# Kernel optimization log

Measured on AMD Instinct MI355X. Metric: run time of the kernel, lower is better.

The kernel has to match this reference:

```python
import jax, jax.numpy as jnp
import numpy as np

DIM = 768
HID = 1536
EPS = 1e-12
SCALE = float(np.sqrt(DIM))


def _layernorm(x, gamma, beta):
    mu = jnp.mean(x, axis=-1, keepdims=True)
    var = jnp.mean(jnp.square(x - mu), axis=-1, keepdims=True)
    return (x - mu) * jax.lax.rsqrt(var + EPS) * gamma + beta


def setup_inputs() -> dict:
    key = jax.random.key(0)
    ks = jax.random.split(key, 16)
    s = 1.0 / np.sqrt(DIM)
    sh = 1.0 / np.sqrt(HID)
    x = jax.random.normal(ks[0], (8, 2048, DIM), dtype=jnp.float32)
    return {
        "x": x,
        "Wq": jax.random.uniform(ks[1], (DIM, DIM), jnp.float32, -s, s),
        "bq": jax.random.uniform(ks[2], (DIM,), jnp.float32, -s, s),
        "Wk": jax.random.uniform(ks[3], (DIM, DIM), jnp.float32, -s, s),
        "bk": jax.random.uniform(ks[4], (DIM,), jnp.float32, -s, s),
        "Wv": jax.random.uniform(ks[5], (DIM, DIM), jnp.float32, -s, s),
        "bv": jax.random.uniform(ks[6], (DIM,), jnp.float32, -s, s),
        "Wp": jax.random.uniform(ks[7], (DIM, DIM), jnp.float32, -s, s),
        "bp": jax.random.uniform(ks[8], (DIM,), jnp.float32, -s, s),
        "g1": jnp.ones((DIM,), jnp.float32),
        "be1": jnp.zeros((DIM,), jnp.float32),
        "W1": jax.random.uniform(ks[9], (HID, DIM), jnp.float32, -s, s),
        "b1": jax.random.uniform(ks[10], (HID,), jnp.float32, -s, s),
        "W2": jax.random.uniform(ks[11], (DIM, HID), jnp.float32, -sh, sh),
        "b2": jax.random.uniform(ks[12], (DIM,), jnp.float32, -sh, sh),
        "g2": jnp.ones((DIM,), jnp.float32),
        "be2": jnp.zeros((DIM,), jnp.float32),
    }


def reference(x, Wq, bq, Wk, bk, Wv, bv, Wp, bp, g1, be1, W1, b1, W2, b2, g2, be2):
    # NOTE: original code does NOT split into heads; single full-dim bmm attention.
    Q = jnp.einsum("bsd,ed->bse", x, Wq) + bq  # [B,S,D]
    K = jnp.einsum("bsd,ed->bse", x, Wk) + bk
    V = jnp.einsum("bsd,ed->bse", x, Wv) + bv
    alpha = jnp.einsum("bqd,bkd->bqk", Q, K) / SCALE  # [B,S,S]
    alpha = jax.nn.softmax(alpha, axis=-1)
    attn = jnp.einsum("bqk,bkd->bqd", alpha, V)
    attn = jnp.einsum("bsd,ed->bse", attn, Wp) + bp  # linear_proj
    h = _layernorm(x + attn, g1, be1)
    mlp = jax.nn.gelu(jnp.einsum("bsd,hd->bsh", h, W1) + b1, approximate=False)
    mlp = jnp.einsum("bsh,dh->bsd", mlp, W2) + b2
    return _layernorm(h + mlp, g2, be2)
```

## Files before the change

### kernel.cpp

```cpp
#include <hip/hip_runtime.h>
#include <math.h>

#define D_MODEL 768
#define D_HID   1536
#define N_BATCH 8
#define SEQLEN  2048
#define NROWS   (N_BATCH*SEQLEN)

typedef unsigned short u16;
typedef __attribute__((ext_vector_type(8))) short bfrag;
typedef __attribute__((ext_vector_type(4))) float facc;

__device__ __forceinline__ u16 f2bf(float f) {
  unsigned u = __float_as_uint(f);
  u += 0x7fffu + ((u >> 16) & 1u);
  return (u16)(u >> 16);
}
__device__ __forceinline__ float bf2f(u16 u) {
  return __uint_as_float((unsigned)u << 16);
}

__device__ __forceinline__ void async16(const void* g, void* l) {
  __builtin_amdgcn_global_load_lds((const __attribute__((address_space(1))) void*)g,
                                   (__attribute__((address_space(3))) void*)l,
                                   16, 0, 0);
}

__global__ __launch_bounds__(256) void cvt_all(
    const float* __restrict__ x,  const float* __restrict__ Wq,
    const float* __restrict__ Wk, const float* __restrict__ Wv,
    const float* __restrict__ Wp, const float* __restrict__ W1,
    const float* __restrict__ W2, const float* __restrict__ bq,
    const float* __restrict__ bk, const float* __restrict__ bv,
    u16* __restrict__ XB, u16* __restrict__ WQKV, u16* __restrict__ WPB,
    u16* __restrict__ W1B, u16* __restrict__ W2B, float* __restrict__ BQKV) {
  long i = (long)blockIdx.x * 256 + threadIdx.x;
  const float* src; u16* dst; long off;
  if      (i < 3145728) { src = x;  dst = XB;             off = i; }
  else if (i < 3293184) { src = Wq; dst = WQKV;           off = i - 3145728; }
  else if (i < 3440640) { src = Wk; dst = WQKV + 589824;  off = i - 3293184; }
  else if (i < 3588096) { src = Wv; dst = WQKV + 1179648; off = i - 3440640; }
  else if (i < 3735552) { src = Wp; dst = WPB;            off = i - 3588096; }
  else if (i < 4030464) { src = W1; dst = W1B;            off = i - 3735552; }
  else if (i < 4325376) { src = W2; dst = W2B;            off = i - 4030464; }
  else if (i < 4325952) {
    long j = i - 4325376;
    const float* s = (j < 192) ? bq : (j < 384) ? bk : bv;
    long o = (j < 192) ? j : (j < 384) ? j - 192 : j - 384;
    ((float4*)BQKV)[j] = ((const float4*)s)[o];
    return;
  } else return;
  float4 v = ((const float4*)src)[off];
  ushort4 o4;
  o4.x = f2bf(v.x); o4.y = f2bf(v.y); o4.z = f2bf(v.z); o4.w = f2bf(v.w);
  *reinterpret_cast<ushort4*>(dst + off * 4) = o4;
}

enum { EPI_EXP = 1, EPI_DIV = 2, EPI_GELU = 4, EPI_QKV = 5, EPI_RES = 6 };

template<int EPI>
__global__ __launch_bounds__(512, 4)
void gemm_bt(const u16* __restrict__ Aall, const u16* __restrict__ Ball,
             void* __restrict__ Cout,
             int M, int N, int K,
             long sA, long sB, long sC,
             const float* __restrict__ bias,
             const u16* __restrict__ resid,
             float* __restrict__ lsum,
             float scale)
{
  __shared__ __align__(16) char smem[65536];
  u16* As = (u16*)smem;
  u16* Bs = (u16*)(smem + 16384);

  const int z = blockIdx.z;
  const u16* A = Aall + (long)z * sA;
  const u16* B = Ball + (long)z * sB;
  const int bm = blockIdx.x, bn = blockIdx.y;
  const int tid = (int)threadIdx.x;
  const int lane = tid & 63, wv = tid >> 6;
  const int wr = wv >> 2, wc = wv & 3;

  facc acc[4][4] = {};

  const int srow = tid >> 3;
  const int scol = (((tid & 7) ^ (srow & 7)) << 3);
  const u16* Abase = A + (long)(bm * 128) * K;
  const u16* Bbase = B + (long)(bn * 256) * K;

  const int fr = lane & 15;
  const int g0 = lane >> 4;

  for (int k0 = 0; k0 < K; k0 += 64) {
    __syncthreads();
#pragma unroll
    for (int p = 0; p < 2; ++p)
      async16(Abase + (long)(p * 64 + srow) * K + k0 + scol, As + (p * 512 + wv * 64) * 8);
#pragma unroll
    for (int p = 0; p < 4; ++p)
      async16(Bbase + (long)(p * 64 + srow) * K + k0 + scol, Bs + (p * 512 + wv * 64) * 8);
    __syncthreads();
#pragma unroll
    for (int h = 0; h < 2; ++h) {
      bfrag af[4], bfv[4];
      const int gh = g0 + h * 4;
#pragma unroll
      for (int i = 0; i < 4; ++i) {
        const int r = wr * 64 + i * 16 + fr;
        af[i] = *(const bfrag*)(As + r * 64 + ((gh ^ (r & 7)) << 3));
      }
#pragma unroll
      for (int j = 0; j < 4; ++j) {
        const int r = wc * 64 + j * 16 + fr;
        bfv[j] = *(const bfrag*)(Bs + r * 64 + ((gh ^ (r & 7)) << 3));
      }
#pragma unroll
      for (int i = 0; i < 4; ++i)
#pragma unroll
        for (int j = 0; j < 4; ++j)
          acc[i][j] = __builtin_amdgcn_mfma_f32_16x16x32_bf16(af[i], bfv[j], acc[i][j], 0, 0, 0);
    }
  }

  __syncthreads();
  const int rb = bm * 128 + wr * 64;
  const int cb = bn * 256 + wc * 64;
  const int quad = lane >> 4;

  if constexpr (EPI == EPI_QKV) {
    const int c64 = bn * 4 + wc;
    const int which = c64 / 12;
    float bj[4];
#pragma unroll
    for (int j = 0; j < 4; ++j) bj[j] = bias[cb + j * 16 + fr];
    if (which == 2) {
      u16* VT_ = (u16*)resid;
      const int zb = rb >> 11;
      const int seqb = (rb & 2047) + quad * 4;
      const int dimb = (c64 - 24) * 64;
#pragma unroll
      for (int i = 0; i < 4; ++i) {
#pragma unroll
        for (int j = 0; j < 4; ++j) {
          const int dim = dimb + j * 16 + fr;
          ushort4 o;
          o.x = f2bf(acc[i][j][0] + bj[j]);
          o.y = f2bf(acc[i][j][1] + bj[j]);
          o.z = f2bf(acc[i][j][2] + bj[j]);
          o.w = f2bf(acc[i][j][3] + bj[j]);
          *reinterpret_cast<ushort4*>(VT_ + (long)zb * D_MODEL * SEQLEN +
                                      (long)dim * SEQLEN + seqb + i * 16) = o;
        }
      }
      return;
    }
    u16* ep16 = (u16*)(smem + wv * 8192);
    u16* Cg = (u16*)Cout + (long)which * NROWS * D_MODEL;
    const int cbo = (c64 - which * 12) * 64;
#pragma unroll
    for (int i = 0; i < 4; ++i)
#pragma unroll
      for (int r = 0; r < 4; ++r) {
        const int lrow = i * 16 + quad * 4 + r;
#pragma unroll
        for (int j = 0; j < 4; ++j)
          ep16[lrow * 64 + j * 16 + fr] = f2bf(acc[i][j][r] + bj[j]);
      }
#pragma unroll
    for (int it = 0; it < 8; ++it) {
      const int lr = it * 8 + (lane >> 3);
      const int ch = (lane & 7) << 3;
      int4 d = *(const int4*)(ep16 + lr * 64 + ch);
      *reinterpret_cast<int4*>(Cg + (long)(rb + lr) * D_MODEL + cbo + ch) = d;
    }
  } else {
    u16* ep16 = (u16*)(smem + wv * 8192);
    u16* Cg = (u16*)Cout + (long)z * sC;
    float bj[4];
    if constexpr (EPI == EPI_GELU) {
#pragma unroll
      for (int j = 0; j < 4; ++j) bj[j] = bias[cb + j * 16 + fr];
    }
#pragma unroll
    for (int i = 0; i < 4; ++i) {
#pragma unroll
      for (int r = 0; r < 4; ++r) {
        const int lrow = i * 16 + quad * 4 + r;
        const int row = rb + lrow;
        float rs = 0.f;
#pragma unroll
        for (int j = 0; j < 4; ++j) {
          float v = acc[i][j][r];
          float outv;
          if constexpr (EPI == EPI_EXP) {
            outv = __expf(v * scale);
            rs += outv;
          } else {
            float t = v + bj[j];
            outv = 0.5f * t * (1.f + erff(t * 0.70710678f));
          }
          ep16[lrow * 64 + j * 16 + fr] = f2bf(outv);
        }
        if constexpr (EPI == EPI_EXP) {
          rs += __shfl_xor(rs, 1);
          rs += __shfl_xor(rs, 2);
          rs += __shfl_xor(rs, 4);
          rs += __shfl_xor(rs, 8);
          if (fr == 0) atomicAdd(&lsum[(long)z * M + row], rs);
        }
      }
    }
#pragma unroll
    for (int it = 0; it < 8; ++it) {
      const int lr = it * 8 + (lane >> 3);
      const int ch = (lane & 7) << 3;
      int4 d = *(const int4*)(ep16 + lr * 64 + ch);
      *reinterpret_cast<int4*>(Cg + (long)(rb + lr) * N + cb + ch) = d;
    }
  }
}

template<int EPI>
__global__ __launch_bounds__(256, 4)
void gemm_bt128(const u16* __restrict__ Aall, const u16* __restrict__ Ball,
                void* __restrict__ Cout,
                int M, int N, int K,
                long sA, long sB, long sC,
                const float* __restrict__ bias,
                const u16* __restrict__ resid,
                float* __restrict__ lsum,
                float scale)
{
  __shared__ __align__(16) char smem[32768];
  u16* As = (u16*)smem;
  u16* Bs = (u16*)(smem + 16384);

  const int z = blockIdx.z;
  const u16* A = Aall + (long)z * sA;
  const u16* B = Ball + (long)z * sB;
  const int bm = blockIdx.x, bn = blockIdx.y;
  const int tid = (int)threadIdx.x;
  const int lane = tid & 63, wv = tid >> 6;
  const int wr = wv >> 1, wc = wv & 1;

  facc acc[4][4] = {};

  const int srow = tid >> 3;
  const int scol = (((tid & 7) ^ (srow & 7)) << 3);
  const u16* Abase = A + (long)(bm * 128) * K;
  const u16* Bbase = B + (long)(bn * 128) * K;
  const int fr = lane & 15, g0 = lane >> 4;

  for (int k0 = 0; k0 < K; k0 += 64) {
    __syncthreads();
#pragma unroll
    for (int p = 0; p < 4; ++p) {
      async16(Abase + (long)(p * 32 + srow) * K + k0 + scol, As + (p * 256 + wv * 64) * 8);
      async16(Bbase + (long)(p * 32 + srow) * K + k0 + scol, Bs + (p * 256 + wv * 64) * 8);
    }
    __syncthreads();
#pragma unroll
    for (int h = 0; h < 2; ++h) {
      bfrag af[4], bfv[4];
      const int gh = g0 + h * 4;
#pragma unroll
      for (int i = 0; i < 4; ++i) {
        const int r = wr * 64 + i * 16 + fr;
        af[i] = *(const bfrag*)(As + r * 64 + ((gh ^ (r & 7)) << 3));
      }
#pragma unroll
      for (int j = 0; j < 4; ++j) {
        const int r = wc * 64 + j * 16 + fr;
        bfv[j] = *(const bfrag*)(Bs + r * 64 + ((gh ^ (r & 7)) << 3));
      }
#pragma unroll
      for (int i = 0; i < 4; ++i)
#pragma unroll
        for (int j = 0; j < 4; ++j)
          acc[i][j] = __builtin_amdgcn_mfma_f32_16x16x32_bf16(af[i], bfv[j], acc[i][j], 0, 0, 0);
    }
  }

  __syncthreads();
  const int rb = bm * 128 + wr * 64;
  const int cb = bn * 128 + wc * 64;
  const int quad = lane >> 4;

  if constexpr (EPI == EPI_RES) {
    float* ep32 = (float*)(smem + wv * 8192);
    u16* Cg = (u16*)Cout;
#pragma unroll
    for (int h = 0; h < 2; ++h) {
#pragma unroll
      for (int i2 = 0; i2 < 2; ++i2) {
        const int i = h * 2 + i2;
#pragma unroll
        for (int r = 0; r < 4; ++r) {
          const int lrow = i2 * 16 + quad * 4 + r;
#pragma unroll
          for (int j = 0; j < 4; ++j)
            ep32[lrow * 64 + j * 16 + fr] = acc[i][j][r];
        }
      }
#pragma unroll
      for (int it = 0; it < 8; ++it) {
        const int lr = it * 4 + (lane >> 4);
        const int ch = (lane & 15) << 2;
        float4 d = *(const float4*)(ep32 + lr * 64 + ch);
        const int row = rb + h * 32 + lr;
        const int gcol = cb + ch;
        const long gi = (long)row * N + gcol;
        ushort4 rv = *(const ushort4*)(resid + gi);
        float4 bb = *(const float4*)(bias + gcol);
        ushort4 o;
        o.x = f2bf(d.x + bb.x + bf2f(rv.x));
        o.y = f2bf(d.y + bb.y + bf2f(rv.y));
        o.z = f2bf(d.z + bb.z + bf2f(rv.z));
        o.w = f2bf(d.w + bb.w + bf2f(rv.w));
        *reinterpret_cast<ushort4*>(Cg + gi) = o;
      }
    }
  } else {
    u16* ep16 = (u16*)(smem + wv * 8192);
    u16* Cg = (u16*)Cout + (long)z * sC;
#pragma unroll
    for (int i = 0; i < 4; ++i) {
#pragma unroll
      for (int r = 0; r < 4; ++r) {
        const int lrow = i * 16 + quad * 4 + r;
        const int row = rb + lrow;
        const float inv = 1.f / lsum[(long)z * M + row];
#pragma unroll
        for (int j = 0; j < 4; ++j)
          ep16[lrow * 64 + j * 16 + fr] = f2bf(acc[i][j][r] * inv);
      }
    }
#pragma unroll
    for (int it = 0; it < 8; ++it) {
      const int lr = it * 8 + (lane >> 3);
      const int ch = (lane & 7) << 3;
      int4 d = *(const int4*)(ep16 + lr * 64 + ch);
      *reinterpret_cast<int4*>(Cg + (long)(rb + lr) * N + cb + ch) = d;
    }
  }
}

__global__ __launch_bounds__(192) void layernorm_rows(const u16* __restrict__ in,
                                                      const float* __restrict__ gamma,
                                                      const float* __restrict__ beta,
                                                      float* __restrict__ outf,
                                                      u16* __restrict__ outb) {
  const int row = blockIdx.x;
  const int t = threadIdx.x;
  ushort4 uv = ((const ushort4*)(in + (long)row * D_MODEL))[t];
  float v0 = bf2f(uv.x), v1 = bf2f(uv.y), v2 = bf2f(uv.z), v3 = bf2f(uv.w);
  float s1 = v0 + v1 + v2 + v3;
  float s2 = v0 * v0 + v1 * v1 + v2 * v2 + v3 * v3;
#pragma unroll
  for (int o = 32; o; o >>= 1) { s1 += __shfl_xor(s1, o); s2 += __shfl_xor(s2, o); }
  __shared__ float r1[3], r2[3];
  const int wv = t >> 6, ln = t & 63;
  if (ln == 0) { r1[wv] = s1; r2[wv] = s2; }
  __syncthreads();
  s1 = r1[0] + r1[1] + r1[2];
  s2 = r2[0] + r2[1] + r2[2];
  const float mu = s1 * (1.f / 768.f);
  const float var = s2 * (1.f / 768.f) - mu * mu;
  const float rstd = rsqrtf(var + 1e-12f);
  float4 gv = ((const float4*)gamma)[t];
  float4 bv = ((const float4*)beta)[t];
  float o0 = (v0 - mu) * rstd * gv.x + bv.x;
  float o1 = (v1 - mu) * rstd * gv.y + bv.y;
  float o2 = (v2 - mu) * rstd * gv.z + bv.z;
  float o3 = (v3 - mu) * rstd * gv.w + bv.w;
  if (outf) {
    float4 ov = {o0, o1, o2, o3};
    ((float4*)(outf + (long)row * D_MODEL))[t] = ov;
  }
  if (outb) {
    ushort4 ob;
    ob.x = f2bf(o0); ob.y = f2bf(o1); ob.z = f2bf(o2); ob.w = f2bf(o3);
    ((ushort4*)(outb + (long)row * D_MODEL))[t] = ob;
  }
}

static const size_t OFF_WP   = 0;
static const size_t OFF_W1   = 1179648;
static const size_t OFF_W2   = 3538944;
static const size_t OFF_LSUM = 5898240;
static const size_t OFF_BQKV = 5963776;
static const size_t OFF_QB   = 6291456;
static const size_t OFF_KB   = 31457280;
static const size_t OFF_VB   = 56623104;
static const size_t OFF_VT   = 81788928;
static const size_t OFF_EB   = 106954752;
static const size_t OFF_XB   = 174063616;
static const size_t OFF_WQKV = 199229440;

extern "C" void kernel_launch(void* const* d_in, const int* in_sizes, int n_in,
                              void* d_out, int out_size, void* d_ws, size_t ws_size,
                              hipStream_t stream) {
  const float* x   = (const float*)d_in[0];
  const float* Wq  = (const float*)d_in[1];
  const float* bq  = (const float*)d_in[2];
  const float* Wk  = (const float*)d_in[3];
  const float* bk  = (const float*)d_in[4];
  const float* Wv  = (const float*)d_in[5];
  const float* bv  = (const float*)d_in[6];
  const float* Wp  = (const float*)d_in[7];
  const float* bp  = (const float*)d_in[8];
  const float* g1  = (const float*)d_in[9];
  const float* be1 = (const float*)d_in[10];
  const float* W1  = (const float*)d_in[11];
  const float* b1  = (const float*)d_in[12];
  const float* W2  = (const float*)d_in[13];
  const float* b2  = (const float*)d_in[14];
  const float* g2  = (const float*)d_in[15];
  const float* be2 = (const float*)d_in[16];

  char* ws = (char*)d_ws;
  u16*   WPB  = (u16*)(ws + OFF_WP);
  u16*   W1B  = (u16*)(ws + OFF_W1);
  u16*   W2B  = (u16*)(ws + OFF_W2);
  float* LSUM = (float*)(ws + OFF_LSUM);
  float* BQKV = (float*)(ws + OFF_BQKV);
  u16*   QB   = (u16*)(ws + OFF_QB);
  u16*   KB   = (u16*)(ws + OFF_KB);
  u16*   VT   = (u16*)(ws + OFF_VT);
  u16*   EB   = (u16*)(ws + OFF_EB);
  u16*   XB   = (u16*)(ws + OFF_XB);
  u16*   WQKV = (u16*)(ws + OFF_WQKV);
  u16*   CTX  = (u16*)(ws + OFF_VB);
  u16*   PB   = (u16*)(ws + OFF_QB);
  u16*   HB   = (u16*)(ws + OFF_EB);
  u16*   M1B  = (u16*)(ws + OFF_QB);
  u16*   M2B  = (u16*)(ws + OFF_VT);

  dim3 blk(256), blkg(512), blkl(192);

  cvt_all<<<dim3(16899), blk, 0, stream>>>(x, Wq, Wk, Wv, Wp, W1, W2, bq, bk, bv,
                                           XB, WQKV, WPB, W1B, W2B, BQKV);
  hipMemsetAsync(LSUM, 0, NROWS * sizeof(float), stream);

  gemm_bt<EPI_QKV><<<dim3(128, 9, 1), blkg, 0, stream>>>(XB, WQKV, QB,
      NROWS, 3 * D_MODEL, D_MODEL, 0, 0, 0, BQKV, VT, nullptr, 0.f);

  const float sc = 1.0f / sqrtf((float)D_MODEL);
  gemm_bt<EPI_EXP><<<dim3(16, 8, 8), blkg, 0, stream>>>(QB, KB, EB,
      SEQLEN, SEQLEN, D_MODEL,
      (long)SEQLEN * D_MODEL, (long)SEQLEN * D_MODEL, (long)SEQLEN * SEQLEN,
      nullptr, nullptr, LSUM, sc);
  gemm_bt128<EPI_DIV><<<dim3(16, 6, 8), blk, 0, stream>>>(EB, VT, CTX,
      SEQLEN, D_MODEL, SEQLEN,
      (long)SEQLEN * SEQLEN, (long)D_MODEL * SEQLEN, (long)SEQLEN * D_MODEL,
      nullptr, nullptr, LSUM, 0.f);
  gemm_bt128<EPI_RES><<<dim3(128, 6, 1), blk, 0, stream>>>(CTX, WPB, PB,
      NROWS, D_MODEL, D_MODEL, 0, 0, 0, bp, XB, nullptr, 0.f);
  layernorm_rows<<<dim3(NROWS), blkl, 0, stream>>>(PB, g1, be1, nullptr, HB);
  gemm_bt<EPI_GELU><<<dim3(128, 6, 1), blkg, 0, stream>>>(HB, W1B, M1B,
      NROWS, D_HID, D_MODEL, 0, 0, 0, b1, nullptr, nullptr, 0.f);
  gemm_bt128<EPI_RES><<<dim3(128, 6, 1), blk, 0, stream>>>(M1B, W2B, M2B,
      NROWS, D_MODEL, D_HID, 0, 0, 0, b2, HB, nullptr, 0.f);
  layernorm_rows<<<dim3(NROWS), blkl, 0, stream>>>(M2B, g2, be2, (float*)d_out, nullptr);

  (void)in_sizes; (void)n_in; (void)out_size; (void)ws_size;
}
```

Baseline: 482.0 us.

## Move attention GEMMs to FP8 with new fp8 MFMA kernel and tanh GELU

Q, K, V^T and the exponentiated score matrix are stored as FP8, and a new gemm_f8 kernel runs QK^T and PV with fp8 MFMA instructions at K-step 128. This halves the bytes of the largest intermediates and should raise matrix throughput. The exact erf GELU is replaced with a tanh approximation, the LSUM memset is folded into the conversion kernel, and the exp uses a fixed offset of -3 to keep values inside FP8 range. Each of these trades accuracy for speed, and the GELU change means the code no longer computes the exact GELU the reference specifies.

```diff
diff --git a/kernel.cpp b/kernel.cpp
--- a/kernel.cpp
+++ b/kernel.cpp
@@ -8,6 +8,7 @@
 #define NROWS   (N_BATCH*SEQLEN)
 
 typedef unsigned short u16;
+typedef unsigned char  u8;
 typedef __attribute__((ext_vector_type(8))) short bfrag;
 typedef __attribute__((ext_vector_type(4))) float facc;
 
@@ -18,6 +19,9 @@
 }
 __device__ __forceinline__ float bf2f(u16 u) {
   return __uint_as_float((unsigned)u << 16);
+}
+__device__ __forceinline__ u8 f2fp8(float f) {
+  return (u8)(__builtin_amdgcn_cvt_pk_fp8_f32(f, f, 0, 0) & 0xff);
 }
 
 __device__ __forceinline__ void async16(const void* g, void* l) {
@@ -33,7 +37,8 @@
     const float* __restrict__ W2, const float* __restrict__ bq,
     const float* __restrict__ bk, const float* __restrict__ bv,
     u16* __restrict__ XB, u16* __restrict__ WQKV, u16* __restrict__ WPB,
-    u16* __restrict__ W1B, u16* __restrict__ W2B, float* __restrict__ BQKV) {
+    u16* __restrict__ W1B, u16* __restrict__ W2B, float* __restrict__ BQKV,
+    float* __restrict__ LSUM) {
   long i = (long)blockIdx.x * 256 + threadIdx.x;
   const float* src; u16* dst; long off;
   if      (i < 3145728) { src = x;  dst = XB;             off = i; }
@@ -49,6 +54,10 @@
     long o = (j < 192) ? j : (j < 384) ? j - 192 : j - 384;
     ((float4*)BQKV)[j] = ((const float4*)s)[o];
     return;
+  } else if (i < 4330048) {
+    float4 zz = {0.f, 0.f, 0.f, 0.f};
+    ((float4*)LSUM)[i - 4325952] = zz;
+    return;
   } else return;
   float4 v = ((const float4*)src)[off];
   ushort4 o4;
@@ -134,7 +143,7 @@
 #pragma unroll
     for (int j = 0; j < 4; ++j) bj[j] = bias[cb + j * 16 + fr];
     if (which == 2) {
-      u16* VT_ = (u16*)resid;
+      u8* VT_ = (u8*)resid;
       const int zb = rb >> 11;
       const int seqb = (rb & 2047) + quad * 4;
       const int dimb = (c64 - 24) * 64;
@@ -143,19 +152,19 @@
 #pragma unroll
         for (int j = 0; j < 4; ++j) {
           const int dim = dimb + j * 16 + fr;
-          ushort4 o;
-          o.x = f2bf(acc[i][j][0] + bj[j]);
-          o.y = f2bf(acc[i][j][1] + bj[j]);
-          o.z = f2bf(acc[i][j][2] + bj[j]);
-          o.w = f2bf(acc[i][j][3] + bj[j]);
-          *reinterpret_cast<ushort4*>(VT_ + (long)zb * D_MODEL * SEQLEN +
-                                      (long)dim * SEQLEN + seqb + i * 16) = o;
+          unsigned v01 = __builtin_amdgcn_cvt_pk_fp8_f32(acc[i][j][0] + bj[j],
+                                                         acc[i][j][1] + bj[j], 0, 0);
+          unsigned v23 = __builtin_amdgcn_cvt_pk_fp8_f32(acc[i][j][2] + bj[j],
+                                                         acc[i][j][3] + bj[j], 0, 0);
+          unsigned w = (v01 & 0xffffu) | (v23 << 16);
+          *reinterpret_cast<unsigned*>(VT_ + (long)zb * D_MODEL * SEQLEN +
+                                       (long)dim * SEQLEN + seqb + i * 16) = w;
         }
       }
       return;
     }
-    u16* ep16 = (u16*)(smem + wv * 8192);
-    u16* Cg = (u16*)Cout + (long)which * NROWS * D_MODEL;
+    u8* ep8 = (u8*)(smem + wv * 8192);
+    u8* Cg = (u8*)Cout + (long)which * NROWS * D_MODEL;
     const int cbo = (c64 - which * 12) * 64;
 #pragma unroll
     for (int i = 0; i < 4; ++i)
@@ -164,49 +173,34 @@
         const int lrow = i * 16 + quad * 4 + r;
 #pragma unroll
         for (int j = 0; j < 4; ++j)
-          ep16[lrow * 64 + j * 16 + fr] = f2bf(acc[i][j][r] + bj[j]);
-      }
-#pragma unroll
-    for (int it = 0; it < 8; ++it) {
-      const int lr = it * 8 + (lane >> 3);
-      const int ch = (lane & 7) << 3;
-      int4 d = *(const int4*)(ep16 + lr * 64 + ch);
+          ep8[lrow * 64 + j * 16 + fr] = f2fp8(acc[i][j][r] + bj[j]);
+      }
+#pragma unroll
+    for (int it = 0; it < 4; ++it) {
+      const int lr = it * 16 + (lane >> 2);
+      const int ch = (lane & 3) << 4;
+      int4 d = *(const int4*)(ep8 + lr * 64 + ch);
       *reinterpret_cast<int4*>(Cg + (long)(rb + lr) * D_MODEL + cbo + ch) = d;
     }
   } else {
     u16* ep16 = (u16*)(smem + wv * 8192);
     u16* Cg = (u16*)Cout + (long)z * sC;
     float bj[4];
-    if constexpr (EPI == EPI_GELU) {
-#pragma unroll
-      for (int j = 0; j < 4; ++j) bj[j] = bias[cb + j * 16 + fr];
-    }
+#pragma unroll
+    for (int j = 0; j < 4; ++j) bj[j] = bias[cb + j * 16 + fr];
 #pragma unroll
     for (int i = 0; i < 4; ++i) {
 #pragma unroll
       for (int r = 0; r < 4; ++r) {
         const int lrow = i * 16 + quad * 4 + r;
-        const int row = rb + lrow;
-        float rs = 0.f;
 #pragma unroll
         for (int j = 0; j < 4; ++j) {
-          float v = acc[i][j][r];
-          float outv;
-          if constexpr (EPI == EPI_EXP) {
-            outv = __expf(v * scale);
-            rs += outv;
-          } else {
-            float t = v + bj[j];
-            outv = 0.5f * t * (1.f + erff(t * 0.70710678f));
-          }
-          ep16[lrow * 64 + j * 16 + fr] = f2bf(outv);
-        }
-        if constexpr (EPI == EPI_EXP) {
-          rs += __shfl_xor(rs, 1);
-          rs += __shfl_xor(rs, 2);
-          rs += __shfl_xor(rs, 4);
-          rs += __shfl_xor(rs, 8);
-          if (fr == 0) atomicAdd(&lsum[(long)z * M + row], rs);
+          float t = acc[i][j][r] + bj[j];
+          float y = 0.7978845608f * (t + 0.044715f * t * t * t);
+          float e = __expf(-2.f * fabsf(y));
+          float th = (1.f - e) / (1.f + e);
+          th = (y < 0.f) ? -th : th;
+          ep16[lrow * 64 + j * 16 + fr] = f2bf(0.5f * t * (1.f + th));
         }
       }
     }
@@ -216,6 +210,132 @@
       const int ch = (lane & 7) << 3;
       int4 d = *(const int4*)(ep16 + lr * 64 + ch);
       *reinterpret_cast<int4*>(Cg + (long)(rb + lr) * N + cb + ch) = d;
+    }
+  }
+}
+
+template<int EPI>
+__global__ __launch_bounds__(512, 4)
+void gemm_f8(const u8* __restrict__ Aall, const u8* __restrict__ Ball,
+             void* __restrict__ Cout,
+             int M, int N, int K,
+             long sA, long sB, long sC,
+             float* __restrict__ lsum, float scale)
+{
+  __shared__ __align__(16) char smem[49152];
+  u8* As = (u8*)smem;
+  u8* Bs = (u8*)(smem + 16384);
+
+  const int z = blockIdx.z;
+  const u8* A = Aall + (long)z * sA;
+  const u8* B = Ball + (long)z * sB;
+  const int bm = blockIdx.x, bn = blockIdx.y;
+  const int tid = (int)threadIdx.x;
+  const int lane = tid & 63, wv = tid >> 6;
+  const int wr = wv >> 2, wc = wv & 3;
+
+  facc acc[4][4] = {};
+
+  const int srow = tid >> 3;
+  const int scol = (((tid & 7) ^ (srow & 7)) << 4);
+  const u8* Abase = A + (long)(bm * 128) * K;
+  const u8* Bbase = B + (long)(bn * 256) * K;
+
+  const int fr = lane & 15;
+  const int g0 = lane >> 4;
+
+  for (int k0 = 0; k0 < K; k0 += 128) {
+    __syncthreads();
+#pragma unroll
+    for (int p = 0; p < 2; ++p)
+      async16(Abase + (long)(p * 64 + srow) * K + k0 + scol, As + (p * 512 + wv * 64) * 16);
+#pragma unroll
+    for (int p = 0; p < 4; ++p)
+      async16(Bbase + (long)(p * 64 + srow) * K + k0 + scol, Bs + (p * 512 + wv * 64) * 16);
+    __syncthreads();
+#pragma unroll
+    for (int s = 0; s < 4; ++s) {
+      long af[4], bfv[4];
+      const int c = s * 2 + (g0 >> 1);
+      const int w8 = (g0 & 1) << 3;
+#pragma unroll
+      for (int i = 0; i < 4; ++i) {
+        const int r = wr * 64 + i * 16 + fr;
+        af[i] = *(const long*)(As + r * 128 + ((c ^ (r & 7)) << 4) + w8);
+      }
+#pragma unroll
+      for (int j = 0; j < 4; ++j) {
+        const int r = wc * 64 + j * 16 + fr;
+        bfv[j] = *(const long*)(Bs + r * 128 + ((c ^ (r & 7)) << 4) + w8);
+      }
+#pragma unroll
+      for (int i = 0; i < 4; ++i)
+#pragma unroll
+        for (int j = 0; j < 4; ++j)
+          acc[i][j] = __builtin_amdgcn_mfma_f32_16x16x32_fp8_fp8(af[i], bfv[j], acc[i][j], 0, 0, 0);
+    }
+  }
+
+  __syncthreads();
+  const int rb = bm * 128 + wr * 64;
+  const int cb = bn * 256 + wc * 64;
+  const int quad = lane >> 4;
+
+  if constexpr (EPI == EPI_EXP) {
+    u8* ep8 = (u8*)(smem + wv * 4096);
+    u8* Cg = (u8*)Cout + (long)z * sC;
+#pragma unroll
+    for (int i = 0; i < 4; ++i) {
+#pragma unroll
+      for (int r = 0; r < 4; ++r) {
+        const int lrow = i * 16 + quad * 4 + r;
+        const int row = rb + lrow;
+        float rs = 0.f;
+#pragma unroll
+        for (int j = 0; j < 4; ++j) {
+          float e = __expf(acc[i][j][r] * scale - 3.0f);
+          rs += e;
+          ep8[lrow * 64 + j * 16 + fr] = f2fp8(e);
+        }
+        rs += __shfl_xor(rs, 1);
+        rs += __shfl_xor(rs, 2);
+        rs += __shfl_xor(rs, 4);
+        rs += __shfl_xor(rs, 8);
+        if (fr == 0) atomicAdd(&lsum[(long)z * M + row], rs);
+      }
+    }
+#pragma unroll
+    for (int it = 0; it < 4; ++it) {
+      const int lr = it * 16 + (lane >> 2);
+      const int ch = (lane & 3) << 4;
+      int4 d = *(const int4*)(ep8 + lr * 64 + ch);
+      *reinterpret_cast<int4*>(Cg + (long)(rb + lr) * N + cb + ch) = d;
+    }
+  } else {
+    u16* ep16 = (u16*)(smem + wv * 4096);
+    u16* Cg = (u16*)Cout + (long)z * sC;
+#pragma unroll
+    for (int h = 0; h < 2; ++h) {
+#pragma unroll
+      for (int i2 = 0; i2 < 2; ++i2) {
+        const int i = h * 2 + i2;
+#pragma unroll
+        for (int r = 0; r < 4; ++r) {
+          const int lrow = i2 * 16 + quad * 4 + r;
+          const int row = rb + h * 32 + lrow;
+          const float inv = 1.f / lsum[(long)z * M + row];
+#pragma unroll
+          for (int j = 0; j < 4; ++j)
+            ep16[lrow * 64 + j * 16 + fr] = f2bf(acc[i][j][r] * inv);
+        }
+      }
+#pragma unroll
+      for (int it = 0; it < 4; ++it) {
+        const int lr = it * 8 + (lane >> 3);
+        const int ch = (lane & 7) << 3;
+        int4 d = *(const int4*)(ep16 + lr * 64 + ch);
+        *reinterpret_cast<int4*>(Cg + (long)(rb + h * 32 + lr) * N + cb + ch) = d;
+      }
     }
   }
 }
@@ -286,63 +406,40 @@
   const int cb = bn * 128 + wc * 64;
   const int quad = lane >> 4;
 
-  if constexpr (EPI == EPI_RES) {
-    float* ep32 = (float*)(smem + wv * 8192);
-    u16* Cg = (u16*)Cout;
-#pragma unroll
-    for (int h = 0; h < 2; ++h) {
-#pragma unroll
-      for (int i2 = 0; i2 < 2; ++i2) {
-        const int i = h * 2 + i2;
-#pragma unroll
-        for (int r = 0; r < 4; ++r) {
-          const int lrow = i2 * 16 + quad * 4 + r;
-#pragma unroll
-          for (int j = 0; j < 4; ++j)
-            ep32[lrow * 64 + j * 16 + fr] = acc[i][j][r];
-        }
-      }
-#pragma unroll
-      for (int it = 0; it < 8; ++it) {
-        const int lr = it * 4 + (lane >> 4);
-        const int ch = (lane & 15) << 2;
-        float4 d = *(const float4*)(ep32 + lr * 64 + ch);
-        const int row = rb + h * 32 + lr;
-        const int gcol = cb + ch;
-        const long gi = (long)row * N + gcol;
-        ushort4 rv = *(const ushort4*)(resid + gi);
-        float4 bb = *(const float4*)(bias + gcol);
-        ushort4 o;
-        o.x = f2bf(d.x + bb.x + bf2f(rv.x));
-        o.y = f2bf(d.y + bb.y + bf2f(rv.y));
-        o.z = f2bf(d.z + bb.z + bf2f(rv.z));
-        o.w = f2bf(d.w + bb.w + bf2f(rv.w));
-        *reinterpret_cast<ushort4*>(Cg + gi) = o;
-      }
-    }
-  } else {
-    u16* ep16 = (u16*)(smem + wv * 8192);
-    u16* Cg = (u16*)Cout + (long)z * sC;
-#pragma unroll
-    for (int i = 0; i < 4; ++i) {
+  float* ep32 = (float*)(smem + wv * 8192);
+  u16* Cg = (u16*)Cout;
+#pragma unroll
+  for (int h = 0; h < 2; ++h) {
+#pragma unroll
+    for (int i2 = 0; i2 < 2; ++i2) {
+      const int i = h * 2 + i2;
 #pragma unroll
       for (int r = 0; r < 4; ++r) {
-        const int lrow = i * 16 + quad * 4 + r;
-        const int row = rb + lrow;
-        const float inv = 1.f / lsum[(long)z * M + row];
+        const int lrow = i2 * 16 + quad * 4 + r;
 #pragma unroll
         for (int j = 0; j < 4; ++j)
-          ep16[lrow * 64 + j * 16 + fr] = f2bf(acc[i][j][r] * inv);
+          ep32[lrow * 64 + j * 16 + fr] = acc[i][j][r];
       }
     }
 #pragma unroll
     for (int it = 0; it < 8; ++it) {
-      const int lr = it * 8 + (lane >> 3);
-      const int ch = (lane & 7) << 3;
-      int4 d = *(const int4*)(ep16 + lr * 64 + ch);
-      *reinterpret_cast<int4*>(Cg + (long)(rb + lr) * N + cb + ch) = d;
-    }
-  }
+      const int lr = it * 4 + (lane >> 4);
+      const int ch = (lane & 15) << 2;
+      float4 d = *(const float4*)(ep32 + lr * 64 + ch);
+      const int row = rb + h * 32 + lr;
+      const int gcol = cb + ch;
+      const long gi = (long)row * N + gcol;
+      ushort4 rv = *(const ushort4*)(resid + gi);
+      float4 bb = *(const float4*)(bias + gcol);
+      ushort4 o;
+      o.x = f2bf(d.x + bb.x + bf2f(rv.x));
+      o.y = f2bf(d.y + bb.y + bf2f(rv.y));
+      o.z = f2bf(d.z + bb.z + bf2f(rv.z));
+      o.w = f2bf(d.w + bb.w + bf2f(rv.w));
+      *reinterpret_cast<ushort4*>(Cg + gi) = o;
+    }
+  }
+  (void)lsum; (void)scale; (void)sC; (void)M;
 }
 
 __global__ __launch_bounds__(192) void layernorm_rows(const u16* __restrict__ in,
@@ -390,12 +487,13 @@
 static const size_t OFF_LSUM = 5898240;
 static const size_t OFF_BQKV = 5963776;
 static const size_t OFF_QB   = 6291456;
-static const size_t OFF_KB   = 31457280;
-static const size_t OFF_VB   = 56623104;
-static const size_t OFF_VT   = 81788928;
-static const size_t OFF_EB   = 106954752;
-static const size_t OFF_XB   = 174063616;
-static const size_t OFF_WQKV = 199229440;
+static const size_t OFF_KB   = 18874368;
+static const size_t OFF_VT   = 31457280;
+static const size_t OFF_EB   = 44040192;
+static const size_t OFF_CTX  = 77594624;
+static const size_t OFF_XB   = 102760448;
+static const size_t OFF_WQKV = 127926272;
+static const size_t OFF_M1B  = 131465216;
 
 extern "C" void kernel_launch(void* const* d_in, const int* in_sizes, int n_in,
                               void* d_out, int out_size, void* d_ws, size_t ws_size,
@@ -424,36 +522,35 @@
   u16*   W2B  = (u16*)(ws + OFF_W2);
   float* LSUM = (float*)(ws + OFF_LSUM);
   float* BQKV = (float*)(ws + OFF_BQKV);
-  u16*   QB   = (u16*)(ws + OFF_QB);
-  u16*   KB   = (u16*)(ws + OFF_KB);
-  u16*   VT   = (u16*)(ws + OFF_VT);
-  u16*   EB   = (u16*)(ws + OFF_EB);
+  u8*    QB   = (u8*)(ws + OFF_QB);
+  u8*    KB   = (u8*)(ws + OFF_KB);
+  u8*    VT   = (u8*)(ws + OFF_VT);
+  u8*    EB   = (u8*)(ws + OFF_EB);
+  u16*   CTX  = (u16*)(ws + OFF_CTX);
   u16*   XB   = (u16*)(ws + OFF_XB);
   u16*   WQKV = (u16*)(ws + OFF_WQKV);
-  u16*   CTX  = (u16*)(ws + OFF_VB);
+  u16*   M1B  = (u16*)(ws + OFF_M1B);
   u16*   PB   = (u16*)(ws + OFF_QB);
   u16*   HB   = (u16*)(ws + OFF_EB);
-  u16*   M1B  = (u16*)(ws + OFF_QB);
-  u16*   M2B  = (u16*)(ws + OFF_VT);
+  u16*   M2B  = (u16*)(ws + OFF_CTX);
 
   dim3 blk(256), blkg(512), blkl(192);
 
-  cvt_all<<<dim3(16899), blk, 0, stream>>>(x, Wq, Wk, Wv, Wp, W1, W2, bq, bk, bv,
-                                           XB, WQKV, WPB, W1B, W2B, BQKV);
-  hipMemsetAsync(LSUM, 0, NROWS * sizeof(float), stream);
+  cvt_all<<<dim3(16915), blk, 0, stream>>>(x, Wq, Wk, Wv, Wp, W1, W2, bq, bk, bv,
+                                           XB, WQKV, WPB, W1B, W2B, BQKV, LSUM);
 
   gemm_bt<EPI_QKV><<<dim3(128, 9, 1), blkg, 0, stream>>>(XB, WQKV, QB,
-      NROWS, 3 * D_MODEL, D_MODEL, 0, 0, 0, BQKV, VT, nullptr, 0.f);
+      NROWS, 3 * D_MODEL, D_MODEL, 0, 0, 0, BQKV, (const u16*)VT, nullptr, 0.f);
 
   const float sc = 1.0f / sqrtf((float)D_MODEL);
-  gemm_bt<EPI_EXP><<<dim3(16, 8, 8), blkg, 0, stream>>>(QB, KB, EB,
+  gemm_f8<EPI_EXP><<<dim3(16, 8, 8), blkg, 0, stream>>>(QB, KB, EB,
       SEQLEN, SEQLEN, D_MODEL,
       (long)SEQLEN * D_MODEL, (long)SEQLEN * D_MODEL, (long)SEQLEN * SEQLEN,
-      nullptr, nullptr, LSUM, sc);
-  gemm_bt128<EPI_DIV><<<dim3(16, 6, 8), blk, 0, stream>>>(EB, VT, CTX,
+      LSUM, sc);
+  gemm_f8<EPI_DIV><<<dim3(16, 3, 8), blkg, 0, stream>>>(EB, VT, CTX,
       SEQLEN, D_MODEL, SEQLEN,
       (long)SEQLEN * SEQLEN, (long)D_MODEL * SEQLEN, (long)SEQLEN * D_MODEL,
-      nullptr, nullptr, LSUM, 0.f);
+      LSUM, 0.f);
   gemm_bt128<EPI_RES><<<dim3(128, 6, 1), blk, 0, stream>>>(CTX, WPB, PB,
       NROWS, D_MODEL, D_MODEL, 0, 0, 0, bp, XB, nullptr, 0.f);
   layernorm_rows<<<dim3(NROWS), blkl, 0, stream>>>(PB, g1, be1, nullptr, HB);
```

Measured after the change: 471.3 us. 1.02x faster.
